# Kernel tuning notes

Measured on AMD Instinct MI355X. Metric: run time of the kernel, lower is better.

The kernel has to match this reference:

```python
import jax, jax.numpy as jnp
import numpy as np


def setup_inputs() -> dict:
    key = jax.random.key(0)
    kx, kw, kr = jax.random.split(key, 3)
    B, N, D = 256, 4096, 64
    X = jax.random.normal(kx, (B, N, D), dtype=jnp.float32)
    W = jax.random.normal(kw, (D,), dtype=jnp.float32)
    b = jnp.zeros((1,), dtype=jnp.float32)
    rankings = jax.random.randint(kr, (B, N), 0, N, dtype=jnp.int64)
    return {"X": X, "W": W, "b": b, "rankings": rankings}


def reference(X, W, b, rankings):
    # Scores: linear score_model with 1D output -> (B, N)
    scores = jnp.einsum("bnd,d->bn", X, W) + b[0]
    # Gather scores in observed ranking order: ranking_scores[b, i] = scores[b, rankings[b, i]]
    ranking_scores = jnp.take_along_axis(scores, rankings, axis=1)
    # Suffix logsumexp: denom[b, i] = logsumexp(ranking_scores[b, i:])
    # Single O(N) reverse scan replaces the original O(N^2) python loop.
    denom = jax.lax.cumlogsumexp(ranking_scores, axis=1, reverse=True)
    # NLL = -(1/B) * sum_b sum_i (s_i - logsumexp(s_i:))
    nll = -jnp.sum(ranking_scores - denom) / X.shape[0]
    return nll
```

## Files before the change

### kernel.cpp

```cpp
#include <hip/hip_runtime.h>
#include <hip/hip_bf16.h>
#include <math.h>

#define BB 256
#define NN 4096
#define DD 64
#define TPB 256
#define CHUNK (NN / TPB)

__global__ __launch_bounds__(256) void scores_kernel(
    const float* __restrict__ X, const float* __restrict__ W,
    const float* __restrict__ bptr, float* __restrict__ scores, int total_rows) {
  __shared__ float4 Wl[16];
  if (threadIdx.x < 16) Wl[threadIdx.x] = ((const float4*)W)[threadIdx.x];
  __syncthreads();
  const float b0 = bptr[0];
  const int lane16 = threadIdx.x & 15;
  const int rowInBlk = threadIdx.x >> 4;
  const float4 w = Wl[lane16];
  const long long stride = (long long)gridDim.x * 16;
  for (long long row = (long long)blockIdx.x * 16 + rowInBlk; row < total_rows; row += stride) {
    const float4* xp = (const float4*)(X + row * DD);
    float4 x = xp[lane16];
    float v = x.x * w.x + x.y * w.y + x.z * w.z + x.w * w.w;
    v += __shfl_xor(v, 1);
    v += __shfl_xor(v, 2);
    v += __shfl_xor(v, 4);
    v += __shfl_xor(v, 8);
    if (lane16 == 0) scores[row] = v + b0;
  }
}

__global__ __launch_bounds__(256) void pl_row_kernel(
    const float* __restrict__ scores, const int* __restrict__ rankings,
    float* __restrict__ rowsum) {
  const int b = blockIdx.x;
  const int t = threadIdx.x;
  const float* srow = scores + (size_t)b * NN;
  const int*   rrow = rankings + (size_t)b * NN;
  const int base = t * CHUNK;

  float xv[CHUNK];
  const int4* rr = (const int4*)(rrow + base);
  #pragma unroll
  for (int q = 0; q < CHUNK / 4; ++q) {
    int4 r4 = rr[q];
    xv[q * 4 + 0] = srow[r4.x];
    xv[q * 4 + 1] = srow[r4.y];
    xv[q * 4 + 2] = srow[r4.z];
    xv[q * 4 + 3] = srow[r4.w];
  }

  float m = -INFINITY, s = 0.f;
  #pragma unroll
  for (int j = CHUNK - 1; j >= 0; --j) {
    float x = xv[j];
    float mn = fmaxf(m, x);
    s = s * __expf(m - mn) + __expf(x - mn);
    m = mn;
  }

  __shared__ float sm[2][TPB], ss[2][TPB];
  sm[0][t] = m; ss[0][t] = s;
  __syncthreads();
  int src = 0;
  for (int off = 1; off < TPB; off <<= 1) {
    float mc = sm[src][t], sc = ss[src][t];
    if (t + off < TPB) {
      float mo = sm[src][t + off], so = ss[src][t + off];
      float mn = fmaxf(mc, mo);
      sc = sc * __expf(mc - mn) + so * __expf(mo - mn);
      mc = mn;
    }
    sm[src ^ 1][t] = mc; ss[src ^ 1][t] = sc;
    __syncthreads();
    src ^= 1;
  }
  float rm, rs;
  if (t == TPB - 1) { rm = -INFINITY; rs = 0.f; }
  else             { rm = sm[src][t + 1]; rs = ss[src][t + 1]; }

  float acc = 0.f;
  #pragma unroll
  for (int j = CHUNK - 1; j >= 0; --j) {
    float x = xv[j];
    float mn = fmaxf(rm, x);
    rs = rs * __expf(rm - mn) + __expf(x - mn);
    rm = mn;
    float denom = rm + __logf(rs);
    acc += x - denom;
  }

  __shared__ float red[TPB];
  red[t] = acc;
  __syncthreads();
  for (int off = TPB / 2; off > 0; off >>= 1) {
    if (t < off) red[t] += red[t + off];
    __syncthreads();
  }
  if (t == 0) rowsum[b] = red[0];
}

__global__ __launch_bounds__(256) void final_kernel(
    const float* __restrict__ rowsum, float* __restrict__ out) {
  const int t = threadIdx.x;
  __shared__ float red[TPB];
  red[t] = (t < BB) ? rowsum[t] : 0.f;
  __syncthreads();
  for (int off = TPB / 2; off > 0; off >>= 1) {
    if (t < off) red[t] += red[t + off];
    __syncthreads();
  }
  if (t == 0) out[0] = -red[0] / (float)BB;
}

extern "C" void kernel_launch(void* const* d_in, const int* in_sizes, int n_in,
                              void* d_out, int out_size, void* d_ws, size_t ws_size,
                              hipStream_t stream) {
  const float* X  = (const float*)d_in[0];
  const float* W  = (const float*)d_in[1];
  const float* bp = (const float*)d_in[2];
  const int*   rk = (const int*)d_in[3];
  float* out = (float*)d_out;

  float* scores = (float*)d_ws;
  float* rowsum = scores + (size_t)BB * NN;

  const int total_rows = BB * NN;
  scores_kernel<<<2048, TPB, 0, stream>>>(X, W, bp, scores, total_rows);
  pl_row_kernel<<<BB, TPB, 0, stream>>>(scores, rk, rowsum);
  final_kernel<<<1, TPB, 0, stream>>>(rowsum, out);
}
```

Baseline: 362.4 us.

## Fuse score GEMV, ranked scan and final reduction into one per-row kernel

Merges the three kernels into one kernel with 1024 threads per batch row. Each block computes its row's scores into shared memory, gathers through the rankings from LDS, and does the suffix logsumexp scan with wave shuffles and a small cross-wave pass. The final mean is accumulated with an atomicAdd after a memset. This removes the global scores round trip and the launch and barrier overhead, at the cost of only 256 blocks streaming 256 MB of X, which may limit memory-bandwidth saturation on a chip with many CUs.

```diff
diff --git a/kernel.cpp b/kernel.cpp
--- a/kernel.cpp
+++ b/kernel.cpp
@@ -1,117 +1,124 @@
 #include <hip/hip_runtime.h>
-#include <hip/hip_bf16.h>
 #include <math.h>
 
 #define BB 256
 #define NN 4096
 #define DD 64
-#define TPB 256
-#define CHUNK (NN / TPB)
+#define TPB 1024
+#define CH (NN / TPB)
 
-__global__ __launch_bounds__(256) void scores_kernel(
+__global__ __launch_bounds__(TPB) void pl_fused_kernel(
     const float* __restrict__ X, const float* __restrict__ W,
-    const float* __restrict__ bptr, float* __restrict__ scores, int total_rows) {
-  __shared__ float4 Wl[16];
-  if (threadIdx.x < 16) Wl[threadIdx.x] = ((const float4*)W)[threadIdx.x];
-  __syncthreads();
+    const float* __restrict__ bptr, const int* __restrict__ rankings,
+    float* __restrict__ out) {
+  __shared__ float srow[NN];
+  __shared__ float wm_s[16], ws_s[16];
+  __shared__ float em_s[16], es_s[16];
+  __shared__ float red_s[16];
+
+  const int b = blockIdx.x;
+  const int t = threadIdx.x;
+  const int lane16 = t & 15;
+  const int g = t >> 4;
+  const int l = t & 63;
+  const int wv = t >> 6;
+
+  const float4 w4 = ((const float4*)W)[lane16];
   const float b0 = bptr[0];
-  const int lane16 = threadIdx.x & 15;
-  const int rowInBlk = threadIdx.x >> 4;
-  const float4 w = Wl[lane16];
-  const long long stride = (long long)gridDim.x * 16;
-  for (long long row = (long long)blockIdx.x * 16 + rowInBlk; row < total_rows; row += stride) {
-    const float4* xp = (const float4*)(X + row * DD);
-    float4 x = xp[lane16];
-    float v = x.x * w.x + x.y * w.y + x.z * w.z + x.w * w.w;
+  const float* Xb = X + (size_t)b * (NN * DD);
+
+  #pragma unroll 4
+  for (int it = 0; it < NN / 64; ++it) {
+    const int n = it * 64 + g;
+    const float4 x = ((const float4*)(Xb + (size_t)n * DD))[lane16];
+    float v = x.x * w4.x + x.y * w4.y + x.z * w4.z + x.w * w4.w;
     v += __shfl_xor(v, 1);
     v += __shfl_xor(v, 2);
     v += __shfl_xor(v, 4);
     v += __shfl_xor(v, 8);
-    if (lane16 == 0) scores[row] = v + b0;
+    if (lane16 == 0) srow[n] = v + b0;
   }
-}
+  __syncthreads();
 
-__global__ __launch_bounds__(256) void pl_row_kernel(
-    const float* __restrict__ scores, const int* __restrict__ rankings,
-    float* __restrict__ rowsum) {
-  const int b = blockIdx.x;
-  const int t = threadIdx.x;
-  const float* srow = scores + (size_t)b * NN;
-  const int*   rrow = rankings + (size_t)b * NN;
-  const int base = t * CHUNK;
+  const int4 r4 = *(const int4*)(rankings + (size_t)b * NN + t * CH);
+  float xv[CH];
+  xv[0] = srow[r4.x]; xv[1] = srow[r4.y]; xv[2] = srow[r4.z]; xv[3] = srow[r4.w];
 
-  float xv[CHUNK];
-  const int4* rr = (const int4*)(rrow + base);
+  float m = xv[CH - 1], s = 1.f;
   #pragma unroll
-  for (int q = 0; q < CHUNK / 4; ++q) {
-    int4 r4 = rr[q];
-    xv[q * 4 + 0] = srow[r4.x];
-    xv[q * 4 + 1] = srow[r4.y];
-    xv[q * 4 + 2] = srow[r4.z];
-    xv[q * 4 + 3] = srow[r4.w];
-  }
-
-  float m = -INFINITY, s = 0.f;
-  #pragma unroll
-  for (int j = CHUNK - 1; j >= 0; --j) {
-    float x = xv[j];
-    float mn = fmaxf(m, x);
-    s = s * __expf(m - mn) + __expf(x - mn);
+  for (int j = CH - 2; j >= 0; --j) {
+    const float mn = fmaxf(m, xv[j]);
+    s = s * __expf(m - mn) + __expf(xv[j] - mn);
     m = mn;
   }
 
-  __shared__ float sm[2][TPB], ss[2][TPB];
-  sm[0][t] = m; ss[0][t] = s;
+  float im = m, is = s;
+  #pragma unroll
+  for (int off = 1; off < 64; off <<= 1) {
+    const float om = __shfl_down(im, off);
+    const float os = __shfl_down(is, off);
+    if (l + off < 64) {
+      const float mn = fmaxf(im, om);
+      is = is * __expf(im - mn) + os * __expf(om - mn);
+      im = mn;
+    }
+  }
+  if (l == 0) { wm_s[wv] = im; ws_s[wv] = is; }
   __syncthreads();
-  int src = 0;
-  for (int off = 1; off < TPB; off <<= 1) {
-    float mc = sm[src][t], sc = ss[src][t];
-    if (t + off < TPB) {
-      float mo = sm[src][t + off], so = ss[src][t + off];
-      float mn = fmaxf(mc, mo);
-      sc = sc * __expf(mc - mn) + so * __expf(mo - mn);
-      mc = mn;
+
+  if (wv == 0) {
+    float am = (l < 16) ? wm_s[l] : -INFINITY;
+    float as = (l < 16) ? ws_s[l] : 0.f;
+    #pragma unroll
+    for (int off = 1; off < 16; off <<= 1) {
+      const float om = __shfl_down(am, off);
+      const float os = __shfl_down(as, off);
+      if (l + off < 16) {
+        const float mn = fmaxf(am, om);
+        as = as * __expf(am - mn) + os * __expf(om - mn);
+        am = mn;
+      }
     }
-    sm[src ^ 1][t] = mc; ss[src ^ 1][t] = sc;
-    __syncthreads();
-    src ^= 1;
+    float em2 = __shfl_down(am, 1);
+    float es2 = __shfl_down(as, 1);
+    if (l == 15) { em2 = -INFINITY; es2 = 0.f; }
+    if (l < 16) { em_s[l] = em2; es_s[l] = es2; }
   }
+  __syncthreads();
+
+  float xm = __shfl_down(im, 1);
+  float xs = __shfl_down(is, 1);
+  if (l == 63) { xm = -INFINITY; xs = 0.f; }
+  const float hm = em_s[wv], hs = es_s[wv];
   float rm, rs;
-  if (t == TPB - 1) { rm = -INFINITY; rs = 0.f; }
-  else             { rm = sm[src][t + 1]; rs = ss[src][t + 1]; }
+  if (xm == -INFINITY)      { rm = hm; rs = hs; }
+  else if (hm == -INFINITY) { rm = xm; rs = xs; }
+  else {
+    const float mn = fmaxf(xm, hm);
+    rs = xs * __expf(xm - mn) + hs * __expf(hm - mn);
+    rm = mn;
+  }
 
   float acc = 0.f;
   #pragma unroll
-  for (int j = CHUNK - 1; j >= 0; --j) {
-    float x = xv[j];
-    float mn = fmaxf(rm, x);
+  for (int j = CH - 1; j >= 0; --j) {
+    const float x = xv[j];
+    const float mn = fmaxf(rm, x);
     rs = rs * __expf(rm - mn) + __expf(x - mn);
     rm = mn;
-    float denom = rm + __logf(rs);
-    acc += x - denom;
+    acc += x - (rm + __logf(rs));
   }
 
-  __shared__ float red[TPB];
-  red[t] = acc;
+  #pragma unroll
+  for (int off = 32; off > 0; off >>= 1) acc += __shfl_xor(acc, off);
+  if (l == 0) red_s[wv] = acc;
   __syncthreads();
-  for (int off = TPB / 2; off > 0; off >>= 1) {
-    if (t < off) red[t] += red[t + off];
-    __syncthreads();
+  if (t == 0) {
+    float tot = 0.f;
+    #pragma unroll
+    for (int i = 0; i < 16; ++i) tot += red_s[i];
+    atomicAdd(out, -tot * (1.f / (float)BB));
   }
-  if (t == 0) rowsum[b] = red[0];
-}
-
-__global__ __launch_bounds__(256) void final_kernel(
-    const float* __restrict__ rowsum, float* __restrict__ out) {
-  const int t = threadIdx.x;
-  __shared__ float red[TPB];
-  red[t] = (t < BB) ? rowsum[t] : 0.f;
-  __syncthreads();
-  for (int off = TPB / 2; off > 0; off >>= 1) {
-    if (t < off) red[t] += red[t + off];
-    __syncthreads();
-  }
-  if (t == 0) out[0] = -red[0] / (float)BB;
 }
 
 extern "C" void kernel_launch(void* const* d_in, const int* in_sizes, int n_in,
@@ -123,11 +130,6 @@
   const int*   rk = (const int*)d_in[3];
   float* out = (float*)d_out;
 
-  float* scores = (float*)d_ws;
-  float* rowsum = scores + (size_t)BB * NN;
-
-  const int total_rows = BB * NN;
-  scores_kernel<<<2048, TPB, 0, stream>>>(X, W, bp, scores, total_rows);
-  pl_row_kernel<<<BB, TPB, 0, stream>>>(scores, rk, rowsum);
-  final_kernel<<<1, TPB, 0, stream>>>(rowsum, out);
+  hipMemsetAsync(out, 0, sizeof(float) * (size_t)out_size, stream);
+  pl_fused_kernel<<<BB, TPB, 0, stream>>>(X, W, bp, rk, out);
 }
```

New measurement: 361.8 us. About the same (-0.2%).
